# Optimization experiments

Hardware: AMD Instinct MI355X
Metric: run time of the kernel (lower is better)

Reference implementation:

```python
import jax, jax.numpy as jnp
import numpy as np

WS = (8, 8)          # window_size -> S = 64
NUM_HEADS = 4
DIM = 128


def _relative_position_index(ws):
    wh, ww = ws
    coords = np.stack(np.meshgrid(np.arange(wh), np.arange(ww), indexing='ij'))  # (2,Wh,Ww)
    cf = coords.reshape(2, -1)                                   # (2, Wh*Ww)
    rel = cf[:, :, None] - cf[:, None, :]                        # (2, S, S)
    rel = rel.transpose(1, 2, 0).astype(np.int64)                # (S, S, 2)
    rel[:, :, 0] += wh - 1
    rel[:, :, 1] += ww - 1
    rel[:, :, 0] *= 2 * ww - 1
    return rel.sum(-1)                                           # (S, S)


def setup_inputs() -> dict:
    key = jax.random.key(0)
    k = jax.random.split(key, 6)
    B, S, N, C = 128, WS[0] * WS[1], 32, DIM
    num_rel = (2 * WS[0] - 1) * (2 * WS[1] - 1)
    return {
        'x': jax.random.normal(k[0], (B, S, N, C), dtype=jnp.float32),
        'qkv_w': jax.random.normal(k[1], (3 * C, C), dtype=jnp.float32) * 0.02,
        'qkv_b': jnp.zeros((3 * C,), dtype=jnp.float32),
        'proj_w': jax.random.normal(k[2], (C, C), dtype=jnp.float32) * 0.02,
        'proj_b': jnp.zeros((C,), dtype=jnp.float32),
        'bias_table': jax.random.normal(k[3], (num_rel, NUM_HEADS), dtype=jnp.float32) * 0.02,
    }


def reference(x, qkv_w, qkv_b, proj_w, proj_b, bias_table):
    B, S, N, C = x.shape
    H = NUM_HEADS
    D = N * C // H                      # effective head dim
    scale = (C // H) ** -0.5            # matches head_dim = dim // num_heads in __init__

    xf = x.reshape(B, S * N, C)
    qkv = xf @ qkv_w.T + qkv_b          # (B, S*N, 3C)
    qkv = qkv.reshape(B, S, 3, H, D).transpose(2, 0, 3, 1, 4)  # (3, B, H, S, D)
    q, k, v = qkv[0], qkv[1], qkv[2]

    rel_idx = jnp.asarray(_relative_position_index(WS))        # (S, S) int
    bias = bias_table[rel_idx.reshape(-1)].reshape(S, S, H).transpose(2, 0, 1)  # (H,S,S)

    attn = jnp.einsum('bhsd,bhtd->bhst', q, k) * scale + bias[None]
    attn = jax.nn.softmax(attn, axis=-1)

    out = jnp.einsum('bhst,bhtd->bhsd', attn, v)               # (B,H,S,D)
    out = out.transpose(0, 2, 1, 3).reshape(B, S * N, C)
    out = out @ proj_w.T + proj_b
    return out.reshape(B, S, N, C)
```

## Files before the change

### kernel.cpp

```cpp
#include <hip/hip_runtime.h>
#include <cmath>


typedef short bf16x8 __attribute__((ext_vector_type(8)));
typedef float f32x4  __attribute__((ext_vector_type(4)));
#define MFMA16 __builtin_amdgcn_mfma_f32_16x16x32_bf16

__device__ __forceinline__ unsigned rne16(float f) {
    unsigned u = __float_as_uint(f);
    return (u + 0x7fffu + ((u >> 16) & 1u)) & 0xffff0000u;
}
__device__ __forceinline__ void cvt8(float4 a, float4 b, bf16x8& H, bf16x8& L) {
    float f[8] = {a.x, a.y, a.z, a.w, b.x, b.y, b.z, b.w};
    #pragma unroll
    for (int i = 0; i < 8; ++i) {
        unsigned r = rne16(f[i]);
        H[i] = (short)(r >> 16);
        float fh = __uint_as_float(r);
        L[i] = (short)(rne16(f[i] - fh) >> 16);
    }
}
__device__ __forceinline__ void cvt8h(float4 a, float4 b, bf16x8& H) {
    float f[8] = {a.x, a.y, a.z, a.w, b.x, b.y, b.z, b.w};
    #pragma unroll
    for (int i = 0; i < 8; ++i) H[i] = (short)(rne16(f[i]) >> 16);
}

__global__ void split_w(const float* __restrict__ qw, unsigned short* __restrict__ wsp) {
    int idx = blockIdx.x * 256 + threadIdx.x;
    if (idx >= 49152) return;
    int j = idx >> 7, c = idx & 127;
    float v = qw[idx];
    unsigned r = rne16(v);
    unsigned rl = rne16(v - __uint_as_float(r));
    int dest = (((j >> 5) * 16 + (c >> 3)) * 32 + (j & 31)) * 8 + (c & 7);
    wsp[dest] = (unsigned short)(r >> 16);
    wsp[49152 + dest] = (unsigned short)(rl >> 16);
}
__global__ void split_pw(const float* __restrict__ pw, unsigned short* __restrict__ pwsp) {
    int idx = blockIdx.x * 256 + threadIdx.x;
    if (idx >= 16384) return;
    int cp = idx >> 7, c = idx & 127;
    float v = pw[idx];
    unsigned r = rne16(v);
    unsigned rl = rne16(v - __uint_as_float(r));
    int dest = ((c >> 3) * 128 + cp) * 8 + (c & 7);
    pwsp[dest] = (unsigned short)(r >> 16);
    pwsp[16384 + dest] = (unsigned short)(rl >> 16);
}

constexpr int A5_QC0 = 0,     A5_KC0 = 16640;
constexpr int A5_QC1 = 33280, A5_KC1 = 49920;
constexpr int A5_P   = 66560;
constexpr int A5_SMA = 74880;
constexpr int A5_SMB = 75392;
constexpr int A5_VC0 = 0,     A5_VC1 = 16640;
constexpr int A5_LDS = 75904;

__global__ __launch_bounds__(512, 4)
void attn_mfma5(const float* __restrict__ x,
                const float* __restrict__ qkv_b,
                const float* __restrict__ bias_table,
                const unsigned short* __restrict__ wsp,
                float* __restrict__ out)
{
    __shared__ __attribute__((aligned(128))) char lds[A5_LDS];
    const int tid = threadIdx.x;
    const int lane = tid & 63;
    const int w = tid >> 6;
    const int l15 = lane & 15, lg = lane >> 4;
    const int qt = w & 3, ch = w >> 2;
    const int rowbase = qt * 16;
    const int b = blockIdx.x >> 2, h = blockIdx.x & 3;
    const float* __restrict__ xb = x + (size_t)b * 262144;
    const float* xrow0 = xb + (size_t)(rowbase + l15) * 4096 + lg * 8;

    bf16x8 aH[4];
    bf16x8 kH[4];
    int cur_na = -1, cur_nk = -1;

    auto loadfrags = [&](int n0, bf16x8 (&H)[4]) {
        const float* p = xrow0 + (size_t)n0 * 128;
        #pragma unroll
        for (int ks = 0; ks < 4; ++ks) {
            float4 a = *(const float4*)(p + ks * 32);
            float4 c = *(const float4*)(p + ks * 32 + 4);
            cvt8h(a, c, H[ks]);
        }
    };

    auto prod64 = [&](const bf16x8 (&H)[4], int j0, f32x4 (&acc)[4]) {
        const unsigned short* wb = wsp + (size_t)(j0 >> 5) * 4096;
        #pragma unroll
        for (int ks = 0; ks < 4; ++ks) {
            #pragma unroll
            for (int ct = 0; ct < 4; ++ct) {
                int gct = ch * 4 + ct;
                int ro = (gct >> 1) * 4096 + ((ks * 4 + lg) * 32 + (gct & 1) * 16 + l15) * 8;
                bf16x8 bh = *(const bf16x8*)(wb + ro);
                acc[ct] = MFMA16(H[ks], bh, acc[ct], 0, 0, 0);
            }
        }
    };

    auto storeP64 = [&](int base, f32x4 (&acc)[4], int j0) {
        #pragma unroll
        for (int ct = 0; ct < 4; ++ct) {
            int d = (ch * 4 + ct) * 16 + l15;
            float bias = qkv_b[j0 + d];
            int dofs = (d >> 3) * 1040 + (d & 7) * 2;
            #pragma unroll
            for (int reg = 0; reg < 4; ++reg) {
                int s = rowbase + lg * 4 + reg;
                *(unsigned short*)(lds + base + dofs + s * 16) =
                    (unsigned short)(rne16(acc[ct][reg] + bias) >> 16);
            }
        }
    };

    auto prodQK = [&](int cc) {
        int remq = h * 1024 + 128 * cc;
        int nq = remq / 384, j0q = remq - nq * 384;
        int remk = 4096 + h * 1024 + 128 * cc;
        int nk = remk / 384, j0k = remk - nk * 384;
        if (nq != cur_na) { loadfrags(nq, aH); cur_na = nq; }
        if (nk != cur_nk) { loadfrags(nk, kH); cur_nk = nk; }
        f32x4 qa[4];
        #pragma unroll
        for (int i = 0; i < 4; ++i) qa[i] = (f32x4){0.f, 0.f, 0.f, 0.f};
        prod64(aH, j0q, qa);
        storeP64((cc & 1) ? A5_QC1 : A5_QC0, qa, j0q);
        f32x4 ka[4];
        #pragma unroll
        for (int i = 0; i < 4; ++i) ka[i] = (f32x4){0.f, 0.f, 0.f, 0.f};
        prod64(kH, j0k, ka);
        storeP64((cc & 1) ? A5_KC1 : A5_KC0, ka, j0k);
    };

    f32x4 accQK[2];
    #pragma unroll
    for (int tt = 0; tt < 2; ++tt) accQK[tt] = (f32x4){0.f, 0.f, 0.f, 0.f};

    prodQK(0);
    __syncthreads();

    for (int cc = 0; cc < 8; ++cc) {
        if (cc < 7) prodQK(cc + 1);

        int qcb = (cc & 1) ? A5_QC1 : A5_QC0;
        int kcb = (cc & 1) ? A5_KC1 : A5_KC0;
        #pragma unroll
        for (int kst = 0; kst < 4; ++kst) {
            int grp = (kst * 4 + lg) * 1040;
            bf16x8 qh = *(const bf16x8*)(lds + qcb + grp + (rowbase + l15) * 16);
            #pragma unroll
            for (int tt = 0; tt < 2; ++tt) {
                int trow = ((ch * 2 + tt) * 16 + l15) * 16;
                bf16x8 kh = *(const bf16x8*)(lds + kcb + grp + trow);
                accQK[tt] = MFMA16(qh, kh, accQK[tt], 0, 0, 0);
            }
        }
        __syncthreads();
    }

    {
        const float scale = 0.17677669529663687f;
        float* smA = (float*)(lds + A5_SMA);
        float* smB = (float*)(lds + A5_SMB);
        float ex[4][2];
        #pragma unroll
        for (int reg = 0; reg < 4; ++reg) {
            int s = rowbase + lg * 4 + reg;
            int i1 = s >> 3, j1 = s & 7;
            float m = -1e30f;
            #pragma unroll
            for (int tt = 0; tt < 2; ++tt) {
                int t = (ch * 2 + tt) * 16 + l15;
                int i2 = t >> 3, j2 = t & 7;
                float L = accQK[tt][reg] * scale
                        + bias_table[((i1 - i2 + 7) * 15 + (j1 - j2 + 7)) * 4 + h];
                ex[reg][tt] = L;
                m = fmaxf(m, L);
            }
            m = fmaxf(m, __shfl_xor(m, 1));
            m = fmaxf(m, __shfl_xor(m, 2));
            m = fmaxf(m, __shfl_xor(m, 4));
            m = fmaxf(m, __shfl_xor(m, 8));
            if (l15 == 0) smA[ch * 64 + s] = m;
        }
        __syncthreads();
        #pragma unroll
        for (int reg = 0; reg < 4; ++reg) {
            int s = rowbase + lg * 4 + reg;
            float mg = fmaxf(smA[s], smA[64 + s]);
            float e0 = __expf(ex[reg][0] - mg);
            float e1 = __expf(ex[reg][1] - mg);
            ex[reg][0] = e0; ex[reg][1] = e1;
            float sum = e0 + e1;
            sum += __shfl_xor(sum, 1);
            sum += __shfl_xor(sum, 2);
            sum += __shfl_xor(sum, 4);
            sum += __shfl_xor(sum, 8);
            if (l15 == 0) smB[ch * 64 + s] = sum;
        }
        __syncthreads();
        #pragma unroll
        for (int reg = 0; reg < 4; ++reg) {
            int s = rowbase + lg * 4 + reg;
            float inv = 1.f / (smB[s] + smB[64 + s]);
            #pragma unroll
            for (int tt = 0; tt < 2; ++tt) {
                int t = (ch * 2 + tt) * 16 + l15;
                int off = (t >> 3) * 1040 + s * 16 + (t & 7) * 2;
                *(unsigned short*)(lds + A5_P + off) =
                    (unsigned short)(rne16(ex[reg][tt] * inv) >> 16);
            }
        }
    }

    cur_na = -1;
    float* ob = out + (size_t)b * 262144;

    auto prodV = [&](int cc) {
        int remv = 8192 + h * 1024 + 128 * cc;
        int nv = remv / 384, j0v = remv - nv * 384;
        if (nv != cur_na) { loadfrags(nv, aH); cur_na = nv; }
        f32x4 va[4];
        #pragma unroll
        for (int i = 0; i < 4; ++i) va[i] = (f32x4){0.f, 0.f, 0.f, 0.f};
        prod64(aH, j0v, va);
        int vcb = (cc & 1) ? A5_VC1 : A5_VC0;
        #pragma unroll
        for (int ct = 0; ct < 4; ++ct) {
            int d = (ch * 4 + ct) * 16 + l15;
            float bias = qkv_b[j0v + d];
            #pragma unroll
            for (int reg = 0; reg < 4; ++reg) {
                int t = rowbase + lg * 4 + reg;
                int off = (t >> 3) * 2080 + d * 16 + (t & 7) * 2;
                *(unsigned short*)(lds + vcb + off) =
                    (unsigned short)(rne16(va[ct][reg] + bias) >> 16);
            }
        }
    };

    prodV(0);
    __syncthreads();

    for (int cc = 0; cc < 8; ++cc) {
        if (cc < 7) prodV(cc + 1);

        int vcb = (cc & 1) ? A5_VC1 : A5_VC0;
        f32x4 o[4];
        #pragma unroll
        for (int i = 0; i < 4; ++i) o[i] = (f32x4){0.f, 0.f, 0.f, 0.f};
        #pragma unroll
        for (int kst = 0; kst < 2; ++kst) {
            bf16x8 pf = *(const bf16x8*)(lds + A5_P + (kst * 4 + lg) * 1040 + (rowbase + l15) * 16);
            int vgrp = (kst * 4 + lg) * 2080;
            #pragma unroll
            for (int dt = 0; dt < 4; ++dt) {
                int drow = ((ch * 4 + dt) * 16 + l15) * 16;
                bf16x8 vh = *(const bf16x8*)(lds + vcb + vgrp + drow);
                o[dt] = MFMA16(pf, vh, o[dt], 0, 0, 0);
            }
        }

        #pragma unroll
        for (int reg = 0; reg < 4; ++reg) {
            int s = rowbase + lg * 4 + reg;
            float* orow = ob + (size_t)(s * 32 + h * 8 + cc) * 128;
            #pragma unroll
            for (int dt = 0; dt < 4; ++dt)
                orow[(ch * 4 + dt) * 16 + l15] = o[dt][reg];
        }
        __syncthreads();
    }
}

__global__ __launch_bounds__(256, 4)
void proj_mfma(const unsigned short* __restrict__ pwsp,
               const float* __restrict__ pb,
               float* __restrict__ io)
{
    const int tid = threadIdx.x;
    const int lane = tid & 63;
    const int w = tid >> 6;
    const int l15 = lane & 15, lg = lane >> 4;
    const size_t rbase = (size_t)blockIdx.x * 64 + w * 16;

    const float* rp = io + (rbase + l15) * 128 + lg * 8;
    bf16x8 aH[4], aL[4];
    #pragma unroll
    for (int ks = 0; ks < 4; ++ks) {
        float4 a = *(const float4*)(rp + ks * 32);
        float4 c = *(const float4*)(rp + ks * 32 + 4);
        cvt8(a, c, aH[ks], aL[ks]);
    }

    f32x4 acc[8];
    #pragma unroll
    for (int i = 0; i < 8; ++i) acc[i] = (f32x4){0.f, 0.f, 0.f, 0.f};

    #pragma unroll
    for (int ks = 0; ks < 4; ++ks) {
        #pragma unroll
        for (int ct = 0; ct < 8; ++ct) {
            int ro = ((ks * 4 + lg) * 128 + ct * 16 + l15) * 8;
            bf16x8 bh = *(const bf16x8*)(pwsp + ro);
            bf16x8 bl = *(const bf16x8*)(pwsp + 16384 + ro);
            acc[ct] = MFMA16(aH[ks], bh, acc[ct], 0, 0, 0);
            acc[ct] = MFMA16(aH[ks], bl, acc[ct], 0, 0, 0);
            acc[ct] = MFMA16(aL[ks], bh, acc[ct], 0, 0, 0);
        }
    }

    #pragma unroll
    for (int ct = 0; ct < 8; ++ct) {
        float bias = pb[ct * 16 + l15];
        #pragma unroll
        for (int reg = 0; reg < 4; ++reg)
            io[(rbase + lg * 4 + reg) * 128 + ct * 16 + l15] = acc[ct][reg] + bias;
    }
}

constexpr int QC_OFF = 0;
constexpr int KC_OFF = 8320;
constexpr int VC_OFF = 24960;
constexpr int P_OFF  = 41856;
constexpr int LDS_TOT = 50176;

__global__ __launch_bounds__(256, 2)
void attn_mfma(const float* __restrict__ x,
               const float* __restrict__ qkv_b,
               const float* __restrict__ bias_table,
               const unsigned short* __restrict__ wsp,
               float* __restrict__ out)
{
    __shared__ __attribute__((aligned(128))) char lds[LDS_TOT];
    const int tid = threadIdx.x;
    const int lane = tid & 63;
    const int w = tid >> 6;
    const int l15 = lane & 15, lg = lane >> 4;
    const int rowbase = 16 * w;
    const int b = blockIdx.x >> 2, h = blockIdx.x & 3;
    const float* __restrict__ xb = x + (size_t)b * 262144;
    const float* xrow0 = xb + ((size_t)(rowbase + l15) * 32) * 128 + lg * 8;

    bf16x8 aH[4], aL[4];
    bf16x8 kH[4], kL[4];
    int cur_na = -1, cur_nk = -1;

    auto loadfrags = [&](int n0, bf16x8 (&H)[4], bf16x8 (&L)[4]) {
        const float* p = xrow0 + (size_t)n0 * 128;
        #pragma unroll
        for (int ks = 0; ks < 4; ++ks) {
            float4 a = *(const float4*)(p + ks * 32);
            float4 c = *(const float4*)(p + ks * 32 + 4);
            cvt8(a, c, H[ks], L[ks]);
        }
    };

    auto mm_band = [&](const bf16x8 (&H)[4], const bf16x8 (&L)[4], int band,
                       f32x4& a0, f32x4& a1) {
        const unsigned short* wb = wsp + (size_t)band * 4096;
        #pragma unroll
        for (int ks = 0; ks < 4; ++ks) {
            int ro = ((ks * 4 + lg) * 32 + l15) * 8;
            bf16x8 b0h = *(const bf16x8*)(wb + ro);
            bf16x8 b0l = *(const bf16x8*)(wb + 49152 + ro);
            bf16x8 b1h = *(const bf16x8*)(wb + ro + 128);
            bf16x8 b1l = *(const bf16x8*)(wb + 49152 + ro + 128);
            a0 = MFMA16(H[ks], b0h, a0, 0, 0, 0);
            a0 = MFMA16(H[ks], b0l, a0, 0, 0, 0);
            a0 = MFMA16(L[ks], b0h, a0, 0, 0, 0);
            a1 = MFMA16(H[ks], b1h, a1, 0, 0, 0);
            a1 = MFMA16(H[ks], b1l, a1, 0, 0, 0);
            a1 = MFMA16(L[ks], b1h, a1, 0, 0, 0);
        }
    };

    auto store_rc = [&](char* base, f32x4 a0, f32x4 a1, float b0, float b1) {
        #pragma unroll
        for (int reg = 0; reg < 4; ++reg) {
            int s = rowbase + lg * 4 + reg;
            {
                float v = a0[reg] + b0;
                int i = l15;
                int off = (i >> 3) * 1040 + s * 16 + (i & 7) * 2;
                unsigned r = rne16(v);
                *(unsigned short*)(base + off) = (unsigned short)(r >> 16);
                *(unsigned short*)(base + 4160 + off) =
                    (unsigned short)(rne16(v - __uint_as_float(r)) >> 16);
            }
            {
                float v = a1[reg] + b1;
                int i = 16 + l15;
                int off = (i >> 3) * 1040 + s * 16 + (i & 7) * 2;
                unsigned r = rne16(v);
                *(unsigned short*)(base + off) = (unsigned short)(r >> 16);
                *(unsigned short*)(base + 4160 + off) =
                    (unsigned short)(rne16(v - __uint_as_float(r)) >> 16);
            }
        }
    };

    f32x4 accQK[4];
    #pragma unroll
    for (int tt = 0; tt < 4; ++tt) accQK[tt] = (f32x4){0.f, 0.f, 0.f, 0.f};

    int buf = 0;
    for (int ccc = 0; ccc < 32; ++ccc) {
        int remq = h * 1024 + 32 * ccc;
        int nq = remq / 384, j0q = remq - nq * 384, bandq = j0q >> 5;
        int remk = 4096 + h * 1024 + 32 * ccc;
        int nk = remk / 384, j0k = remk - nk * 384, bandk = j0k >> 5;
        if (nq != cur_na) { loadfrags(nq, aH, aL); cur_na = nq; }
        if (nk != cur_nk) { loadfrags(nk, kH, kL); cur_nk = nk; }

        f32x4 q0 = (f32x4){0.f,0.f,0.f,0.f}, q1 = (f32x4){0.f,0.f,0.f,0.f};
        mm_band(aH, aL, bandq, q0, q1);
        store_rc(lds + QC_OFF, q0, q1, qkv_b[j0q + l15], qkv_b[j0q + 16 + l15]);

        f32x4 k0 = (f32x4){0.f,0.f,0.f,0.f}, k1 = (f32x4){0.f,0.f,0.f,0.f};
        mm_band(kH, kL, bandk, k0, k1);
        store_rc(lds + KC_OFF + buf * 8320, k0, k1, qkv_b[j0k + l15], qkv_b[j0k + 16 + l15]);

        __syncthreads();

        const char* qc = lds + QC_OFF + lg * 1040 + (rowbase + l15) * 16;
        bf16x8 qah = *(const bf16x8*)qc;
        bf16x8 qal = *(const bf16x8*)(qc + 4160);
        #pragma unroll
        for (int tt = 0; tt < 4; ++tt) {
            const char* kc = lds + KC_OFF + buf * 8320 + lg * 1040 + (tt * 16 + l15) * 16;
            bf16x8 kbh = *(const bf16x8*)kc;
            bf16x8 kbl = *(const bf16x8*)(kc + 4160);
            accQK[tt] = MFMA16(qah, kbh, accQK[tt], 0, 0, 0);
            accQK[tt] = MFMA16(qah, kbl, accQK[tt], 0, 0, 0);
            accQK[tt] = MFMA16(qal, kbh, accQK[tt], 0, 0, 0);
        }
        buf ^= 1;
    }

    {
        const float scale = 0.17677669529663687f;
        #pragma unroll
        for (int reg = 0; reg < 4; ++reg) {
            int s = rowbase + lg * 4 + reg;
            int i1 = s >> 3, j1 = s & 7;
            float Lv[4];
            float m = -1e30f;
            #pragma unroll
            for (int tt = 0; tt < 4; ++tt) {
                int t = tt * 16 + l15;
                int i2 = t >> 3, j2 = t & 7;
                float L = accQK[tt][reg] * scale
                        + bias_table[((i1 - i2 + 7) * 15 + (j1 - j2 + 7)) * 4 + h];
                Lv[tt] = L;
                m = fmaxf(m, L);
            }
            m = fmaxf(m, __shfl_xor(m, 1));
            m = fmaxf(m, __shfl_xor(m, 2));
            m = fmaxf(m, __shfl_xor(m, 4));
            m = fmaxf(m, __shfl_xor(m, 8));
            float sum = 0.f;
            #pragma unroll
            for (int tt = 0; tt < 4; ++tt) { Lv[tt] = __expf(Lv[tt] - m); sum += Lv[tt]; }
            sum += __shfl_xor(sum, 1);
            sum += __shfl_xor(sum, 2);
            sum += __shfl_xor(sum, 4);
            sum += __shfl_xor(sum, 8);
            float inv = 1.f / sum;
            #pragma unroll
            for (int tt = 0; tt < 4; ++tt) {
                int t = tt * 16 + l15;
                int off = (t >> 3) * 1040 + s * 16 + (t & 7) * 2;
                *(unsigned short*)(lds + P_OFF + off) = (unsigned short)(rne16(Lv[tt] * inv) >> 16);
            }
        }
    }

    cur_na = -1;
    int bufv = 0;
    float* ob = out + (size_t)b * 262144;
    for (int ccc = 0; ccc < 32; ++ccc) {
        int remv = 8192 + h * 1024 + 32 * ccc;
        int nv = remv / 384, j0v = remv - nv * 384, bandv = j0v >> 5;
        if (nv != cur_na) { loadfrags(nv, aH, aL); cur_na = nv; }

        f32x4 v0 = (f32x4){0.f,0.f,0.f,0.f}, v1 = (f32x4){0.f,0.f,0.f,0.f};
        mm_band(aH, aL, bandv, v0, v1);
        {
            char* base = lds + VC_OFF + bufv * 8448;
            float b0 = qkv_b[j0v + l15], b1 = qkv_b[j0v + 16 + l15];
            #pragma unroll
            for (int reg = 0; reg < 4; ++reg) {
                int t = rowbase + lg * 4 + reg;
                {
                    float v = v0[reg] + b0;
                    int i = l15;
                    int off = (t >> 3) * 528 + i * 16 + (t & 7) * 2;
                    unsigned r = rne16(v);
                    *(unsigned short*)(base + off) = (unsigned short)(r >> 16);
                    *(unsigned short*)(base + 4224 + off) =
                        (unsigned short)(rne16(v - __uint_as_float(r)) >> 16);
                }
                {
                    float v = v1[reg] + b1;
                    int i = 16 + l15;
                    int off = (t >> 3) * 528 + i * 16 + (t & 7) * 2;
                    unsigned r = rne16(v);
                    *(unsigned short*)(base + off) = (unsigned short)(r >> 16);
                    *(unsigned short*)(base + 4224 + off) =
                        (unsigned short)(rne16(v - __uint_as_float(r)) >> 16);
                }
            }
        }
        __syncthreads();

        f32x4 o0 = (f32x4){0.f,0.f,0.f,0.f}, o1 = (f32x4){0.f,0.f,0.f,0.f};
        #pragma unroll
        for (int ks = 0; ks < 2; ++ks) {
            bf16x8 pf = *(const bf16x8*)(lds + P_OFF + (ks * 4 + lg) * 1040 + (rowbase + l15) * 16);
            const char* vb = lds + VC_OFF + bufv * 8448 + (ks * 4 + lg) * 528;
            bf16x8 v0h = *(const bf16x8*)(vb + l15 * 16);
            bf16x8 v0l = *(const bf16x8*)(vb + 4224 + l15 * 16);
            bf16x8 v1h = *(const bf16x8*)(vb + (16 + l15) * 16);
            bf16x8 v1l = *(const bf16x8*)(vb + 4224 + (16 + l15) * 16);
            o0 = MFMA16(pf, v0h, o0, 0, 0, 0);
            o0 = MFMA16(pf, v0l, o0, 0, 0, 0);
            o1 = MFMA16(pf, v1h, o1, 0, 0, 0);
            o1 = MFMA16(pf, v1l, o1, 0, 0, 0);
        }
        bufv ^= 1;

        #pragma unroll
        for (int reg = 0; reg < 4; ++reg) {
            int s = rowbase + lg * 4 + reg;
            {
                int d = 32 * ccc + l15;
                ob[(s * 32 + h * 8 + (d >> 7)) * 128 + (d & 127)] = o0[reg];
            }
            {
                int d = 32 * ccc + 16 + l15;
                ob[(s * 32 + h * 8 + (d >> 7)) * 128 + (d & 127)] = o1[reg];
            }
        }
    }
}

constexpr int LDS_B = 128 * 132 + 64 * 132;

__global__ __launch_bounds__(256, 1)
void proj_inplace(const float* __restrict__ pw,
                  const float* __restrict__ pb,
                  float* __restrict__ io)
{
    __shared__ float lds[LDS_B];
    float* pwt  = lds;
    float* rows = lds + 128 * 132;
    const int tid = threadIdx.x;

    for (int idx = tid; idx < 128 * 128; idx += 256) {
        const int c = idx >> 7, cp = idx & 127;
        pwt[cp * 132 + c] = pw[idx];
    }
    const int rb = tid >> 5;
    const int cg = tid & 31;
    const float4 pbv = *(const float4*)(pb + cg * 4);

    for (int it = 0; it < 8; ++it) {
        const size_t base = ((size_t)blockIdx.x * 8 + it) * 64;
        __syncthreads();
        for (int f = tid; f < 64 * 32; f += 256) {
            const int r = f >> 5, c4 = f & 31;
            *(float4*)(rows + r * 132 + c4 * 4) =
                *(const float4*)(io + (base + r) * 128 + c4 * 4);
        }
        __syncthreads();
        float acc[8][4] = {};
        #pragma unroll 2
        for (int cp = 0; cp < 128; ++cp) {
            const float4 wv = *(const float4*)(pwt + cp * 132 + cg * 4);
            #pragma unroll
            for (int rr = 0; rr < 8; ++rr) {
                const float xv = rows[(rb * 8 + rr) * 132 + cp];
                acc[rr][0] += xv * wv.x;
                acc[rr][1] += xv * wv.y;
                acc[rr][2] += xv * wv.z;
                acc[rr][3] += xv * wv.w;
            }
        }
        #pragma unroll
        for (int rr = 0; rr < 8; ++rr) {
            float4 o;
            o.x = acc[rr][0] + pbv.x;
            o.y = acc[rr][1] + pbv.y;
            o.z = acc[rr][2] + pbv.z;
            o.w = acc[rr][3] + pbv.w;
            *(float4*)(io + (base + rb * 8 + rr) * 128 + cg * 4) = o;
        }
    }
}

extern "C" void kernel_launch(void* const* d_in, const int* in_sizes, int n_in,
                              void* d_out, int out_size, void* d_ws, size_t ws_size,
                              hipStream_t stream)
{
    const float* x          = (const float*)d_in[0];
    const float* qkv_w      = (const float*)d_in[1];
    const float* qkv_b      = (const float*)d_in[2];
    const float* proj_w     = (const float*)d_in[3];
    const float* proj_b     = (const float*)d_in[4];
    const float* bias_table = (const float*)d_in[5];
    float* out = (float*)d_out;

    if (ws_size >= 262144 && d_ws != nullptr) {
        unsigned short* wsp = (unsigned short*)d_ws;
        split_w<<<dim3(192), dim3(256), 0, stream>>>(qkv_w, wsp);
        split_pw<<<dim3(64), dim3(256), 0, stream>>>(proj_w, wsp + 98304);
        attn_mfma5<<<dim3(512), dim3(512), 0, stream>>>(x, qkv_b, bias_table, wsp, out);
        proj_mfma<<<dim3(4096), dim3(256), 0, stream>>>(wsp + 98304, proj_b, out);
    } else if (ws_size >= 196608 && d_ws != nullptr) {
        unsigned short* wsp = (unsigned short*)d_ws;
        split_w<<<dim3(192), dim3(256), 0, stream>>>(qkv_w, wsp);
        attn_mfma<<<dim3(512), dim3(256), 0, stream>>>(x, qkv_b, bias_table, wsp, out);
        proj_inplace<<<dim3(512), dim3(256), 0, stream>>>(proj_w, proj_b, out);
    }
}
```

Measured before the change: 192.5 us.

## Fuse output projection into attention kernel epilogue via LDS staging

The attention kernel no longer writes its per-chunk output to global memory for a separate projection kernel to read back. It splits each output into bf16 hi/lo parts, stages them in LDS, and runs the projection GEMM with three-term split-bf16 MFMAs against the pre-split proj weights before adding the bias and storing. This removes one kernel launch and a full read-write round trip of the output tensor. In exchange it adds an extra barrier per chunk and more per-block compute and register pressure, and it loads the projection weights from global memory inside the loop.

```diff
diff --git a/kernel.cpp b/kernel.cpp
--- a/kernel.cpp
+++ b/kernel.cpp
@@ -55,13 +55,16 @@
 constexpr int A5_SMA = 74880;
 constexpr int A5_SMB = 75392;
 constexpr int A5_VC0 = 0,     A5_VC1 = 16640;
+constexpr int A5_PSH = 33280, A5_PSL = 49920;
 constexpr int A5_LDS = 75904;
 
 __global__ __launch_bounds__(512, 4)
-void attn_mfma5(const float* __restrict__ x,
+void attn_mfma7(const float* __restrict__ x,
                 const float* __restrict__ qkv_b,
                 const float* __restrict__ bias_table,
                 const unsigned short* __restrict__ wsp,
+                const unsigned short* __restrict__ pwsp,
+                const float* __restrict__ pb,
                 float* __restrict__ out)
 {
     __shared__ __attribute__((aligned(128))) char lds[A5_LDS];
@@ -267,12 +270,49 @@
         }
 
         #pragma unroll
-        for (int reg = 0; reg < 4; ++reg) {
-            int s = rowbase + lg * 4 + reg;
-            float* orow = ob + (size_t)(s * 32 + h * 8 + cc) * 128;
-            #pragma unroll
-            for (int dt = 0; dt < 4; ++dt)
-                orow[(ch * 4 + dt) * 16 + l15] = o[dt][reg];
+        for (int dt = 0; dt < 4; ++dt) {
+            int c = (ch * 4 + dt) * 16 + l15;
+            int cofs = (c >> 3) * 1040 + (c & 7) * 2;
+            #pragma unroll
+            for (int reg = 0; reg < 4; ++reg) {
+                int s = rowbase + lg * 4 + reg;
+                float v = o[dt][reg];
+                unsigned r = rne16(v);
+                *(unsigned short*)(lds + A5_PSH + cofs + s * 16) = (unsigned short)(r >> 16);
+                *(unsigned short*)(lds + A5_PSL + cofs + s * 16) =
+                    (unsigned short)(rne16(v - __uint_as_float(r)) >> 16);
+            }
+        }
+        __syncthreads();
+
+        f32x4 p[4];
+        #pragma unroll
+        for (int i = 0; i < 4; ++i) p[i] = (f32x4){0.f, 0.f, 0.f, 0.f};
+        #pragma unroll
+        for (int ks = 0; ks < 4; ++ks) {
+            int grp = (ks * 4 + lg) * 1040;
+            bf16x8 pah = *(const bf16x8*)(lds + A5_PSH + grp + (rowbase + l15) * 16);
+            bf16x8 pal = *(const bf16x8*)(lds + A5_PSL + grp + (rowbase + l15) * 16);
+            #pragma unroll
+            for (int ct = 0; ct < 4; ++ct) {
+                int ro = ((ks * 4 + lg) * 128 + (ch * 4 + ct) * 16 + l15) * 8;
+                bf16x8 bh = *(const bf16x8*)(pwsp + ro);
+                bf16x8 bl = *(const bf16x8*)(pwsp + 16384 + ro);
+                p[ct] = MFMA16(pah, bh, p[ct], 0, 0, 0);
+                p[ct] = MFMA16(pah, bl, p[ct], 0, 0, 0);
+                p[ct] = MFMA16(pal, bh, p[ct], 0, 0, 0);
+            }
+        }
+
+        #pragma unroll
+        for (int ct = 0; ct < 4; ++ct) {
+            int cp = (ch * 4 + ct) * 16 + l15;
+            float bias = pb[cp];
+            #pragma unroll
+            for (int reg = 0; reg < 4; ++reg) {
+                int s = rowbase + lg * 4 + reg;
+                ob[(size_t)(s * 32 + h * 8 + cc) * 128 + cp] = p[ct][reg] + bias;
+            }
         }
         __syncthreads();
     }
@@ -618,10 +658,11 @@
 
     if (ws_size >= 262144 && d_ws != nullptr) {
         unsigned short* wsp = (unsigned short*)d_ws;
+        unsigned short* pwsp = wsp + 98304;
         split_w<<<dim3(192), dim3(256), 0, stream>>>(qkv_w, wsp);
-        split_pw<<<dim3(64), dim3(256), 0, stream>>>(proj_w, wsp + 98304);
-        attn_mfma5<<<dim3(512), dim3(512), 0, stream>>>(x, qkv_b, bias_table, wsp, out);
-        proj_mfma<<<dim3(4096), dim3(256), 0, stream>>>(wsp + 98304, proj_b, out);
+        split_pw<<<dim3(64), dim3(256), 0, stream>>>(proj_w, pwsp);
+        attn_mfma7<<<dim3(512), dim3(512), 0, stream>>>(x, qkv_b, bias_table, wsp,
+                                                        pwsp, proj_b, out);
     } else if (ws_size >= 196608 && d_ws != nullptr) {
         unsigned short* wsp = (unsigned short*)d_ws;
         split_w<<<dim3(192), dim3(256), 0, stream>>>(qkv_w, wsp);
```

Result: slower. 263.3 us (+36.8%).
